# Performance work log

Measured on AMD Instinct MI355X. Metric: run time of the kernel, lower is better.

The kernel has to match this reference:

```python
import jax, jax.numpy as jnp
import numpy as np
from jax.scipy.ndimage import map_coordinates

IMG = 256
N_ANG = 50
BATCH = 4
N_CNN = 32
IN_CH = 2


def _circle_mask(S):
    c = (S - 1) / 2.0
    yy, xx = jnp.meshgrid(jnp.arange(S, dtype=jnp.float32), jnp.arange(S, dtype=jnp.float32), indexing='ij')
    return (((yy - c) ** 2 + (xx - c) ** 2) <= (S / 2.0) ** 2).astype(jnp.float32)


def radon_forward(img, angles):
    # img [B,1,S,S] -> sinogram [B,1,A,S]; parallel-beam, clip_to_circle=True
    S = img.shape[-1]
    c = (S - 1) / 2.0
    img = img * _circle_mask(S)
    t = jnp.arange(S, dtype=jnp.float32) - c        # integration coord
    s = jnp.arange(S, dtype=jnp.float32) - c        # detector coord
    cos = jnp.cos(angles)[:, None, None]
    sin = jnp.sin(angles)[:, None, None]
    x = s[None, None, :] * cos - t[None, :, None] * sin   # [A,S,S]
    y = s[None, None, :] * sin + t[None, :, None] * cos
    coords = jnp.stack([y + c, x + c])                    # [2,A,S,S] (row, col)
    samp = jax.vmap(lambda im: map_coordinates(im, coords, order=1, mode='constant', cval=0.0))(img[:, 0])  # [B,A,S,S]
    return samp.sum(axis=2)[:, None]                      # sum over ray param -> [B,1,A,S]


def filter_sinogram(sino):
    # Ram-Lak FFT filter with zero-padding + FBP normalization
    S = sino.shape[-1]
    A = sino.shape[2]
    P = max(64, int(2 ** np.ceil(np.log2(2 * S))))
    f = jnp.fft.rfft(jnp.pad(sino, ((0, 0), (0, 0), (0, 0), (0, P - S))), axis=-1)
    ramp = 2.0 * jnp.fft.rfftfreq(P).astype(jnp.float32)
    out = jnp.fft.irfft(f * ramp, n=P, axis=-1)[..., :S]
    return out * (np.pi / (2.0 * A))


def radon_backprojection(sino, angles):
    # sino [B,1,A,S] -> image [B,1,S,S]
    B, _, A, S = sino.shape
    c = (S - 1) / 2.0
    yy, xx = jnp.meshgrid(jnp.arange(S, dtype=jnp.float32) - c, jnp.arange(S, dtype=jnp.float32) - c, indexing='ij')
    cos = jnp.cos(angles)[:, None, None]
    sin = jnp.sin(angles)[:, None, None]
    det = xx[None] * cos + yy[None] * sin + c             # [A,S,S] detector coord
    sino2 = sino[:, 0]                                    # [B,A,S]

    def interp_one(sino_a, idx):
        # sino_a [B,S], idx [S,S] -> [B,S,S] linear interp, zero outside
        i0 = jnp.clip(jnp.floor(idx).astype(jnp.int32), 0, S - 2)
        w = idx - i0
        v = sino_a[:, i0] * (1.0 - w) + sino_a[:, i0 + 1] * w
        valid = (idx >= 0.0) & (idx <= S - 1.0)
        return jnp.where(valid, v, 0.0)

    bp = jax.vmap(interp_one, in_axes=(1, 0))(sino2, det).sum(axis=0)  # [B,S,S]
    return (bp * _circle_mask(S))[:, None]


def conv2d(x, w, b):
    y = jax.lax.conv_general_dilated(x, w, (1, 1), 'SAME', dimension_numbers=('NCHW', 'OIHW', 'NCHW'))
    return y + b[None, :, None, None]


def setup_inputs() -> dict:
    key = jax.random.key(0)
    ks = jax.random.split(key, 10)
    angles = jnp.asarray(np.linspace(0, np.pi, N_ANG, endpoint=False), dtype=jnp.float32)
    return {
        'x_sinogram': jax.random.normal(ks[0], (BATCH, 1, N_ANG, IMG), dtype=jnp.float32),
        'y_img_prev': jax.random.normal(ks[1], (BATCH, 1, IMG, IMG), dtype=jnp.float32),
        'y_img_concat_prev': jax.random.normal(ks[2], (BATCH, 1, IMG, IMG), dtype=jnp.float32),
        'angles': angles,
        'step': jnp.float32(1.0),
        'w1': jax.random.normal(ks[3], (N_CNN, IN_CH, 3, 3), dtype=jnp.float32) * 0.1,
        'b1': jnp.zeros((N_CNN,), dtype=jnp.float32),
        'w2': jax.random.normal(ks[4], (N_CNN, N_CNN, 3, 3), dtype=jnp.float32) * 0.1,
        'b2': jnp.zeros((N_CNN,), dtype=jnp.float32),
        'w3': jax.random.normal(ks[5], (1, N_CNN, 3, 3), dtype=jnp.float32) * 0.1,
        'b3': jnp.zeros((1,), dtype=jnp.float32),
    }


def reference(x_sinogram, y_img_prev, y_img_concat_prev, angles, step, w1, b1, w2, b2, w3, b3):
    Ay = radon_forward(y_img_prev, angles)                 # [B,1,A,S]
    diff = Ay - x_sinogram
    filt = filter_sinogram(diff)
    fbp = radon_backprojection(filt, angles)               # [B,1,S,S]
    y_img_update = y_img_prev + step * fbp
    y_cat = jnp.concatenate([y_img_update, y_img_concat_prev], axis=1)  # [B,2,S,S]
    h = jax.nn.relu(conv2d(y_cat, w1, b1))
    h = jax.nn.relu(conv2d(h, w2, b2))
    y_img = conv2d(h, w3, b3)
    return (y_img, y_img_update)
```

## Files before the change

### kernel.cpp

```cpp
#include <hip/hip_runtime.h>
#include <math.h>

#define IMGS 256
#define NANG 50
#define BATCH 4
#define NCNN 32
#define PIX (IMGS*IMGS)
#define NPIX (BATCH*PIX)

#define PROW 258
#define PPIX (PROW*PROW)
#define PB   (PPIX*NCNN)

#define OFF_FILT  0
#define OFF_W2BF  51200
#define OFF_H1P   55808

static constexpr double PI_D = 3.14159265358979323846;

typedef unsigned short u16;
typedef unsigned int   u32;
typedef unsigned long long u64;
typedef __bf16 bfrag __attribute__((ext_vector_type(8)));
typedef float  ffrag __attribute__((ext_vector_type(4)));

__device__ __forceinline__ u16 f2bf(float f) {
    u32 u = __float_as_uint(f);
    u += 0x7fffu + ((u >> 16) & 1u);
    return (u16)(u >> 16);
}

#define RPITCH_D 131
__global__ __launch_bounds__(1024) void k_A(const float* __restrict__ angles,
                                            const float* __restrict__ yprev,
                                            const float* __restrict__ xsino,
                                            const float* __restrict__ w2,
                                            float* __restrict__ ws) {
    __shared__ u16 limg[258 * 262];
    __shared__ float spart[1024];
    __shared__ float staps[512];
    __shared__ float srow[256];
    int tid = threadIdx.x;
    int gid = blockIdx.x;
    if (gid >= 200) {
        int i = (gid - 200) * 1024 + tid;
        if (i < 9216) {
            int t = i >> 10, oc = (i >> 5) & 31, ic = i & 31;
            ((u16*)(ws + OFF_W2BF))[i] = f2bf(w2[(oc * 32 + ic) * 9 + t]);
        }
        return;
    }
    u32* l32 = (u32*)limg;
    int ra = gid;
    int a = ra % NANG, b = ra / NANG;

    if (tid < 511) {
        int d = tid - 255;
        int n = d < 0 ? -d : d;
        double g;
        if (n == 0) {
            g = 0.5;
        } else {
            double th = PI_D * (double)n / 256.0;
            double S = (256.0 * cos(255.0 * th) - 255.0 * cos(256.0 * th) - 1.0)
                       / (2.0 * (1.0 - cos(th)));
            double sign = (n & 1) ? -1.0 : 1.0;
            g = (sign + S / 128.0) / 512.0;
        }
        staps[tid] = (float)(g * PI_D / 100.0);
    }

    for (int z = tid; z < 772; z += 1024) {
        int addr;
        if (z < 258)      addr = z * RPITCH_D;
        else if (z < 516) addr = (z - 258) * RPITCH_D + 129;
        else if (z < 644) addr = (z - 516) + 1;
        else              addr = 257 * RPITCH_D + (z - 644) + 1;
        l32[addr] = 0;
    }
    const float* __restrict__ src = yprev + b * PIX;
    for (int idx = tid; idx < 16384; idx += 1024) {
        int r = idx >> 6, c4 = (idx & 63) << 2;
        float4 v = *(const float4*)(src + r * 256 + c4);
        float di = (float)r - 127.5f;
        float rr = di * di;
        float d0 = (float)c4 - 127.5f;
        v.x = (rr + d0 * d0 <= 16384.0f) ? v.x : 0.0f;
        v.y = (rr + (d0 + 1.0f) * (d0 + 1.0f) <= 16384.0f) ? v.y : 0.0f;
        v.z = (rr + (d0 + 2.0f) * (d0 + 2.0f) <= 16384.0f) ? v.z : 0.0f;
        v.w = (rr + (d0 + 3.0f) * (d0 + 3.0f) <= 16384.0f) ? v.w : 0.0f;
        u32 p0 = (u32)f2bf(v.x) | ((u32)f2bf(v.y) << 16);
        u32 p1 = (u32)f2bf(v.z) | ((u32)f2bf(v.w) << 16);
        int dw = (r + 1) * RPITCH_D + (c4 >> 1) + 1;
        l32[dw] = p0; l32[dw + 1] = p1;
    }
    __syncthreads();

    float a_ = angles[a];
    float cs = cosf(a_), sn = sinf(a_);
    int s = tid & 255, q = tid >> 8;
    float sc = (float)s - 127.5f;
    float t0c = 64.0f * (float)q - 127.5f;
    float rowv = sc * sn + t0c * cs + 127.5f;
    float colv = sc * cs - t0c * sn + 127.5f;
    float acc = 0.0f;
    #pragma unroll 4
    for (int it = 0; it < 64; ++it) {
        float fr = floorf(rowv), fc = floorf(colv);
        float wr = rowv - fr, wc = colv - fc;
        int i0 = (int)fr, j0 = (int)fc;
        bool valid = (rowv > -1.0f) & (rowv < 256.0f) & (colv > -1.0f) & (colv < 256.0f);
        int i0c = min(max(i0, -1), 255);
        int j0c = min(max(j0, -1), 255);
        int ca = j0c + 2;
        int ka = ca >> 1;
        int sh = (ca & 1) << 4;
        int dw = (i0c + 1) * RPITCH_D + ka;
        u32 A = l32[dw],            C = l32[dw + 1];
        u32 B = l32[dw + RPITCH_D], D = l32[dw + RPITCH_D + 1];
        u32 top = (u32)((((u64)C << 32) | (u64)A) >> sh);
        u32 bot = (u32)((((u64)D << 32) | (u64)B) >> sh);
        float tl = __uint_as_float(top << 16);
        float tr_ = __uint_as_float(top & 0xffff0000u);
        float bl = __uint_as_float(bot << 16);
        float br = __uint_as_float(bot & 0xffff0000u);
        float tv = tl + (tr_ - tl) * wc;
        float bv = bl + (br - bl) * wc;
        float sv = tv + (bv - tv) * wr;
        acc += valid ? sv : 0.0f;
        rowv += cs; colv -= sn;
    }
    spart[tid] = acc;
    __syncthreads();
    if (tid < 256)
        srow[tid] = spart[tid] + spart[tid + 256] + spart[tid + 512] + spart[tid + 768]
                    - xsino[ra * 256 + tid];
    __syncthreads();
    {
        float fa = 0.0f;
        int m0 = q * 64;
        #pragma unroll 8
        for (int m = m0; m < m0 + 64; ++m) fa += srow[m] * staps[s - m + 255];
        spart[tid] = fa;
    }
    __syncthreads();
    if (tid < 256)
        ws[OFF_FILT + ra * 256 + tid] =
            spart[tid] + spart[tid + 256] + spart[tid + 512] + spart[tid + 768];
}

__global__ __launch_bounds__(512, 4) void k_B(const float* __restrict__ angles,
                                              const float* __restrict__ yprev,
                                              const float* __restrict__ yconc,
                                              const float* __restrict__ stepp,
                                              const float* __restrict__ w1,
                                              const float* __restrict__ b1,
                                              float* __restrict__ ws,
                                              float* __restrict__ dout) {
    __shared__ float sf[NANG * 256];
    __shared__ float supd[6][258];
    __shared__ float sy2[6][258];
    __shared__ float scs[NANG], ssn[NANG];
    int tid = threadIdx.x;
    int b = blockIdx.x >> 6, tile = blockIdx.x & 63;
    int y0 = tile << 2;

    for (int idx = tid; idx < NANG * 256; idx += 512)
        sf[idx] = ws[OFF_FILT + b * (NANG * 256) + idx];
    if (tid < NANG) {
        float a_ = angles[tid];
        scs[tid] = cosf(a_); ssn[tid] = sinf(a_);
    }
    if (tid < 12) supd[tid >> 1][(tid & 1) * 257] = 0.0f;
    for (int idx = tid; idx < 6 * 258; idx += 512) {
        int r = idx / 258, x = idx % 258;
        int iy = y0 - 1 + r, ix = x - 1;
        sy2[r][x] = ((unsigned)iy < 256u && (unsigned)ix < 256u)
                        ? yconc[b * PIX + iy * 256 + ix] : 0.0f;
    }
    {
        if (tid < 272) {
            int px_i = tile * 17 + (tid >> 4), dw = tid & 15;
            if (px_i < 1028) {
                int y, x;
                if (px_i < 516) { y = (px_i < 258) ? 0 : 257; x = px_i % 258; }
                else            { int j = px_i - 516; y = 1 + (j >> 1); x = (j & 1) * 257; }
                u32* p = (u32*)((u16*)(ws + OFF_H1P) + b * PB + (y * PROW + x) * NCNN);
                p[dw] = 0;
            }
        }
    }
    __syncthreads();

    float step = stepp[0];
    {
        int j = tid & 255, r0 = tid >> 8;
        float xx = (float)j - 127.5f;
        float yy0 = (float)(y0 - 1 + r0) - 127.5f;
        float acc[3] = {0.0f, 0.0f, 0.0f};
        for (int a = 0; a < NANG; ++a) {
            float cs = scs[a], sn = ssn[a];
            float sn2 = sn + sn;
            float f0 = xx * cs + yy0 * sn + 127.5f;
            float idxf[3] = {f0, f0 + sn2, f0 + sn2 + sn2};
            #pragma unroll
            for (int k = 0; k < 3; ++k) {
                float fl = floorf(idxf[k]);
                int i0 = (int)fl;
                i0 = min(max(i0, 0), 254);
                float w = idxf[k] - (float)i0;
                float v = sf[a * 256 + i0] * (1.0f - w) + sf[a * 256 + i0 + 1] * w;
                acc[k] += (idxf[k] >= 0.0f && idxf[k] <= 255.0f) ? v : 0.0f;
            }
        }
        #pragma unroll
        for (int k = 0; k < 3; ++k) {
            int r = r0 + 2 * k;
            int iy = y0 - 1 + r;
            float val = 0.0f;
            if ((unsigned)iy < 256u) {
                float yy = (float)iy - 127.5f;
                float m = (xx * xx + yy * yy <= 16384.0f) ? 1.0f : 0.0f;
                val = yprev[b * PIX + iy * 256 + j] + step * acc[k] * m;
                if (r >= 1 && r <= 4)
                    dout[NPIX + b * PIX + iy * 256 + j] = val;
            }
            supd[r][j + 1] = val;
        }
    }
    __syncthreads();

    {
        int wave = tid >> 6, lane = tid & 63;
        int oc0 = wave * 4;
        float W[72];
        const float4* wsrc = (const float4*)(w1 + oc0 * 18);
        #pragma unroll
        for (int i = 0; i < 18; ++i) ((float4*)W)[i] = wsrc[i];
        float bb0 = b1[oc0], bb1 = b1[oc0 + 1], bb2 = b1[oc0 + 2], bb3 = b1[oc0 + 3];
        u16* h1base = (u16*)(ws + OFF_H1P) + b * PB;
        for (int it = 0; it < 16; ++it) {
            int px = it * 64 + lane;
            int rr = px >> 8, x = px & 255;
            int oy = y0 + rr;
            float v[18];
            #pragma unroll
            for (int ky = 0; ky < 3; ++ky)
                #pragma unroll
                for (int kx = 0; kx < 3; ++kx) {
                    v[ky * 3 + kx]     = supd[rr + ky][x + kx];
                    v[9 + ky * 3 + kx] = sy2[rr + ky][x + kx];
                }
            float a0 = bb0, a1 = bb1, a2 = bb2, a3 = bb3;
            #pragma unroll
            for (int t = 0; t < 18; ++t) {
                a0 += v[t] * W[t];
                a1 += v[t] * W[18 + t];
                a2 += v[t] * W[36 + t];
                a3 += v[t] * W[54 + t];
            }
            u32 p0 = (u32)f2bf(fmaxf(a0, 0.0f)) | ((u32)f2bf(fmaxf(a1, 0.0f)) << 16);
            u32 p1 = (u32)f2bf(fmaxf(a2, 0.0f)) | ((u32)f2bf(fmaxf(a3, 0.0f)) << 16);
            u32* op = (u32*)(h1base + ((oy + 1) * PROW + (x + 1)) * NCNN + oc0);
            op[0] = p0; op[1] = p1;
        }
    }
}

#define H2PITCH 34
__global__ __launch_bounds__(1024) void k_C(const float* __restrict__ b2,
                                            const float* __restrict__ w3,
                                            const float* __restrict__ b3,
                                            float* __restrict__ ws,
                                            float* __restrict__ dout) {
    __shared__ u16 sh2[6 * 258 * H2PITCH];
    __shared__ u32 swp[9 * 16];
    u32* l32 = (u32*)sh2;
    int tid = threadIdx.x;
    int b = blockIdx.x >> 6, tile = blockIdx.x & 63;
    int y0 = tile << 2;

    if (tid < 144) {
        int t = tid >> 4, kd = tid & 15;
        swp[tid] = (u32)f2bf(w3[(2 * kd) * 9 + t]) | ((u32)f2bf(w3[(2 * kd + 1) * 9 + t]) << 16);
    }
    if (tid < 204) {
        int r = tid / 34, rem = tid % 34;
        int col = (rem < 17) ? 0 : 257, dw = rem % 17;
        l32[(r * 258 + col) * 17 + dw] = 0;
    }
    #pragma unroll
    for (int r = 0; r < 6; ++r) {
        int hy = y0 - 1 + r;
        if (hy < 0 || hy > 255)
            for (int idx = tid; idx < 258 * 17; idx += 1024)
                l32[r * 258 * 17 + idx] = 0;
    }
    __syncthreads();

    const u16* __restrict__ w2bf = (const u16*)(ws + OFF_W2BF);
    const u16* __restrict__ h1b  = (const u16*)(ws + OFF_H1P) + b * PB;
    int wave = tid >> 6, lane = tid & 63;
    int m = lane & 15, quad = lane >> 4;
    bfrag Bf[9][2];
    #pragma unroll
    for (int t = 0; t < 9; ++t) {
        const u16* wp = w2bf + t * 1024 + m * 32 + quad * 8;
        Bf[t][0] = *(const bfrag*)(wp);
        Bf[t][1] = *(const bfrag*)(wp + 16 * 32);
    }
    float bias0 = b2[m], bias1 = b2[m + 16];
    #pragma unroll
    for (int k = 0; k < 6; ++k) {
        int tl = wave + (k << 4);
        int ridx = tl >> 4, xt = tl & 15;
        int hy = y0 - 1 + ridx;
        bool valid = (unsigned)hy < 256u;
        int hyc = min(max(hy, 0), 255);
        int xs = xt << 4;
        ffrag c0 = {0.f, 0.f, 0.f, 0.f}, c1 = {0.f, 0.f, 0.f, 0.f};
        #pragma unroll
        for (int g = 0; g < 3; ++g) {
            bfrag Af[3];
            #pragma unroll
            for (int tt = 0; tt < 3; ++tt) {
                int t = g * 3 + tt;
                int ty = t / 3, tx = t % 3;
                Af[tt] = *(const bfrag*)(h1b + ((hyc + ty) * PROW + xs + m + tx) * NCNN + quad * 8);
            }
            #pragma unroll
            for (int tt = 0; tt < 3; ++tt) {
                c0 = __builtin_amdgcn_mfma_f32_16x16x32_bf16(Af[tt], Bf[g * 3 + tt][0], c0, 0, 0, 0);
                c1 = __builtin_amdgcn_mfma_f32_16x16x32_bf16(Af[tt], Bf[g * 3 + tt][1], c1, 0, 0, 0);
            }
        }
        if (valid) {
            #pragma unroll
            for (int r = 0; r < 4; ++r) {
                int px = xs + quad * 4 + r;
                u16* op = sh2 + (ridx * 258 + px + 1) * H2PITCH;
                op[m]      = f2bf(fmaxf(c0[r] + bias0, 0.0f));
                op[m + 16] = f2bf(fmaxf(c1[r] + bias1, 0.0f));
            }
        }
    }
    __syncthreads();

    {
        uint4 WP[9];
        #pragma unroll
        for (int t = 0; t < 9; ++t) WP[t] = ((const uint4*)swp)[t * 4 + 0],
                                    WP[t] = *(const uint4*)(swp + t * 16);
        u32 Wd[36];
        #pragma unroll
        for (int i = 0; i < 36; ++i) Wd[i] = swp[(i / 4) * 16 + (i & 3)];
        (void)WP;
        int rr = tid >> 8, x = tid & 255;
        int oy = y0 + rr;
        float acc = b3[0];
        #pragma unroll
        for (int ky = 0; ky < 3; ++ky) {
            #pragma unroll
            for (int cx = 0; cx < 3; ++cx) {
                int t = ky * 3 + cx;
                const u32* q = l32 + ((rr + ky) * 258 + x + cx) * 17;
                #pragma unroll
                for (int kd = 0; kd < 16; ++kd) {
                    u32 hv = q[kd];
                    u32 wv = (kd < 4) ? Wd[t * 4 + kd] : swp[t * 16 + kd];
                    float h0 = __uint_as_float(hv << 16);
                    float h1 = __uint_as_float(hv & 0xffff0000u);
                    float w0 = __uint_as_float(wv << 16);
                    float w1_ = __uint_as_float(wv & 0xffff0000u);
                    acc += h0 * w0 + h1 * w1_;
                }
            }
        }
        dout[b * PIX + oy * 256 + x] = acc;
    }
}

extern "C" void kernel_launch(void* const* d_in, const int* in_sizes, int n_in,
                              void* d_out, int out_size, void* d_ws, size_t ws_size,
                              hipStream_t stream) {
    const float* xsino  = (const float*)d_in[0];
    const float* yprev  = (const float*)d_in[1];
    const float* yconc  = (const float*)d_in[2];
    const float* angles = (const float*)d_in[3];
    const float* stepp  = (const float*)d_in[4];
    const float* w1 = (const float*)d_in[5];
    const float* b1 = (const float*)d_in[6];
    const float* w2 = (const float*)d_in[7];
    const float* b2 = (const float*)d_in[8];
    const float* w3 = (const float*)d_in[9];
    const float* b3 = (const float*)d_in[10];
    float* out = (float*)d_out;
    float* ws  = (float*)d_ws;

    k_A<<<209, 1024, 0, stream>>>(angles, yprev, xsino, w2, ws);
    k_B<<<BATCH * 64, 512, 0, stream>>>(angles, yprev, yconc, stepp, w1, b1, ws, out);
    k_C<<<BATCH * 64, 1024, 0, stream>>>(b2, w3, b3, ws, out);
}
```

Measured before the change: 157.6 us.

## Remap radon rays to 8x8 wave tiles and halve row tiles in k_B/k_C

In k_A, each wave now handles a patch of 16 detector bins by 8 ray offsets, walking two interleaved ray segments with stride 8 and reducing through wave shuffles. This gives more local LDS access and removes the 4-way partial-sum reduction in shared memory. k_B and k_C now use 2-row tiles with twice as many blocks, and k_C drops to 512 threads. k_C also gets a restructured MFMA loop that prefetches A fragments row by row, plus float4 staging of the filtered sinogram and removal of dead weight-register code. Smaller tiles raise parallelism and occupancy but add more redundant halo rows and backprojection work per output row.

```diff
diff --git a/kernel.cpp b/kernel.cpp
--- a/kernel.cpp
+++ b/kernel.cpp
@@ -31,11 +31,11 @@
 }
 
 #define RPITCH_D 131
-__global__ __launch_bounds__(1024) void k_A(const float* __restrict__ angles,
-                                            const float* __restrict__ yprev,
-                                            const float* __restrict__ xsino,
-                                            const float* __restrict__ w2,
-                                            float* __restrict__ ws) {
+__global__ __launch_bounds__(1024, 4) void k_A(const float* __restrict__ angles,
+                                               const float* __restrict__ yprev,
+                                               const float* __restrict__ xsino,
+                                               const float* __restrict__ w2,
+                                               float* __restrict__ ws) {
     __shared__ u16 limg[258 * 262];
     __shared__ float spart[1024];
     __shared__ float staps[512];
@@ -98,45 +98,62 @@
 
     float a_ = angles[a];
     float cs = cosf(a_), sn = sinf(a_);
-    int s = tid & 255, q = tid >> 8;
-    float sc = (float)s - 127.5f;
-    float t0c = 64.0f * (float)q - 127.5f;
-    float rowv = sc * sn + t0c * cs + 127.5f;
-    float colv = sc * cs - t0c * sn + 127.5f;
-    float acc = 0.0f;
+    int lane = tid & 63, w = tid >> 6;
+    int s8 = lane & 7, t8 = lane >> 3;
+    int sA = w * 16 + s8;
+    float scA = (float)sA - 127.5f;
+    float tc0 = (float)t8 - 127.5f;
+    float rowA = scA * sn + tc0 * cs + 127.5f;
+    float colA = scA * cs - tc0 * sn + 127.5f;
+    float rowB = rowA + 8.0f * sn;
+    float colB = colA + 8.0f * cs;
+    float cs8 = 8.0f * cs, sn8 = 8.0f * sn;
+    float accA = 0.0f, accB = 0.0f;
     #pragma unroll 4
-    for (int it = 0; it < 64; ++it) {
-        float fr = floorf(rowv), fc = floorf(colv);
-        float wr = rowv - fr, wc = colv - fc;
-        int i0 = (int)fr, j0 = (int)fc;
-        bool valid = (rowv > -1.0f) & (rowv < 256.0f) & (colv > -1.0f) & (colv < 256.0f);
-        int i0c = min(max(i0, -1), 255);
-        int j0c = min(max(j0, -1), 255);
-        int ca = j0c + 2;
-        int ka = ca >> 1;
-        int sh = (ca & 1) << 4;
-        int dw = (i0c + 1) * RPITCH_D + ka;
-        u32 A = l32[dw],            C = l32[dw + 1];
-        u32 B = l32[dw + RPITCH_D], D = l32[dw + RPITCH_D + 1];
-        u32 top = (u32)((((u64)C << 32) | (u64)A) >> sh);
-        u32 bot = (u32)((((u64)D << 32) | (u64)B) >> sh);
-        float tl = __uint_as_float(top << 16);
-        float tr_ = __uint_as_float(top & 0xffff0000u);
-        float bl = __uint_as_float(bot << 16);
-        float br = __uint_as_float(bot & 0xffff0000u);
-        float tv = tl + (tr_ - tl) * wc;
-        float bv = bl + (br - bl) * wc;
-        float sv = tv + (bv - tv) * wr;
-        acc += valid ? sv : 0.0f;
-        rowv += cs; colv -= sn;
-    }
-    spart[tid] = acc;
+    for (int j = 0; j < 32; ++j) {
+        #pragma unroll
+        for (int hh = 0; hh < 2; ++hh) {
+            float rowv = hh ? rowB : rowA;
+            float colv = hh ? colB : colA;
+            float fr = floorf(rowv), fc = floorf(colv);
+            float wr = rowv - fr, wc = colv - fc;
+            int i0 = (int)fr, j0 = (int)fc;
+            bool valid = (rowv > -1.0f) & (rowv < 256.0f) & (colv > -1.0f) & (colv < 256.0f);
+            int i0c = min(max(i0, -1), 255);
+            int j0c = min(max(j0, -1), 255);
+            int ca = j0c + 2;
+            int ka = ca >> 1;
+            int sh = (ca & 1) << 4;
+            int dw = (i0c + 1) * RPITCH_D + ka;
+            u32 A = l32[dw],            C = l32[dw + 1];
+            u32 B = l32[dw + RPITCH_D], D = l32[dw + RPITCH_D + 1];
+            u32 top = (u32)((((u64)C << 32) | (u64)A) >> sh);
+            u32 bot = (u32)((((u64)D << 32) | (u64)B) >> sh);
+            float tl = __uint_as_float(top << 16);
+            float tr_ = __uint_as_float(top & 0xffff0000u);
+            float bl = __uint_as_float(bot << 16);
+            float br = __uint_as_float(bot & 0xffff0000u);
+            float tv = tl + (tr_ - tl) * wc;
+            float bv = bl + (br - bl) * wc;
+            float sv = tv + (bv - tv) * wr;
+            sv = valid ? sv : 0.0f;
+            if (hh) accB += sv; else accA += sv;
+        }
+        rowA += cs8; colA -= sn8; rowB += cs8; colB -= sn8;
+    }
+    accA += __shfl_xor(accA, 8, 64);
+    accA += __shfl_xor(accA, 16, 64);
+    accA += __shfl_xor(accA, 32, 64);
+    accB += __shfl_xor(accB, 8, 64);
+    accB += __shfl_xor(accB, 16, 64);
+    accB += __shfl_xor(accB, 32, 64);
+    if (t8 == 0) { spart[sA] = accA; spart[sA + 8] = accB; }
     __syncthreads();
     if (tid < 256)
-        srow[tid] = spart[tid] + spart[tid + 256] + spart[tid + 512] + spart[tid + 768]
-                    - xsino[ra * 256 + tid];
+        srow[tid] = spart[tid] - xsino[ra * 256 + tid];
     __syncthreads();
     {
+        int s = tid & 255, q = tid >> 8;
         float fa = 0.0f;
         int m0 = q * 64;
         #pragma unroll 8
@@ -158,36 +175,37 @@
                                               float* __restrict__ ws,
                                               float* __restrict__ dout) {
     __shared__ float sf[NANG * 256];
-    __shared__ float supd[6][258];
-    __shared__ float sy2[6][258];
+    __shared__ float supd[4][258];
+    __shared__ float sy2[4][258];
     __shared__ float scs[NANG], ssn[NANG];
     int tid = threadIdx.x;
-    int b = blockIdx.x >> 6, tile = blockIdx.x & 63;
-    int y0 = tile << 2;
-
-    for (int idx = tid; idx < NANG * 256; idx += 512)
-        sf[idx] = ws[OFF_FILT + b * (NANG * 256) + idx];
+    int b = blockIdx.x >> 7, tile = blockIdx.x & 127;
+    int y0 = tile << 1;
+
+    {
+        const float4* s4 = (const float4*)(ws + OFF_FILT + b * (NANG * 256));
+        float4* d4 = (float4*)sf;
+        for (int idx = tid; idx < NANG * 64; idx += 512) d4[idx] = s4[idx];
+    }
     if (tid < NANG) {
         float a_ = angles[tid];
         scs[tid] = cosf(a_); ssn[tid] = sinf(a_);
     }
-    if (tid < 12) supd[tid >> 1][(tid & 1) * 257] = 0.0f;
-    for (int idx = tid; idx < 6 * 258; idx += 512) {
+    if (tid < 8) supd[tid >> 1][(tid & 1) * 257] = 0.0f;
+    for (int idx = tid; idx < 4 * 258; idx += 512) {
         int r = idx / 258, x = idx % 258;
         int iy = y0 - 1 + r, ix = x - 1;
         sy2[r][x] = ((unsigned)iy < 256u && (unsigned)ix < 256u)
                         ? yconc[b * PIX + iy * 256 + ix] : 0.0f;
     }
-    {
-        if (tid < 272) {
-            int px_i = tile * 17 + (tid >> 4), dw = tid & 15;
-            if (px_i < 1028) {
-                int y, x;
-                if (px_i < 516) { y = (px_i < 258) ? 0 : 257; x = px_i % 258; }
-                else            { int j = px_i - 516; y = 1 + (j >> 1); x = (j & 1) * 257; }
-                u32* p = (u32*)((u16*)(ws + OFF_H1P) + b * PB + (y * PROW + x) * NCNN);
-                p[dw] = 0;
-            }
+    if (tid < 144) {
+        int px_i = tile * 9 + (tid >> 4), dw = tid & 15;
+        if (px_i < 1028) {
+            int y, x;
+            if (px_i < 516) { y = (px_i < 258) ? 0 : 257; x = px_i % 258; }
+            else            { int j = px_i - 516; y = 1 + (j >> 1); x = (j & 1) * 257; }
+            u32* p = (u32*)((u16*)(ws + OFF_H1P) + b * PB + (y * PROW + x) * NCNN);
+            p[dw] = 0;
         }
     }
     __syncthreads();
@@ -197,14 +215,14 @@
         int j = tid & 255, r0 = tid >> 8;
         float xx = (float)j - 127.5f;
         float yy0 = (float)(y0 - 1 + r0) - 127.5f;
-        float acc[3] = {0.0f, 0.0f, 0.0f};
+        float acc[2] = {0.0f, 0.0f};
+        #pragma unroll 5
         for (int a = 0; a < NANG; ++a) {
             float cs = scs[a], sn = ssn[a];
-            float sn2 = sn + sn;
             float f0 = xx * cs + yy0 * sn + 127.5f;
-            float idxf[3] = {f0, f0 + sn2, f0 + sn2 + sn2};
+            float idxf[2] = {f0, f0 + sn + sn};
             #pragma unroll
-            for (int k = 0; k < 3; ++k) {
+            for (int k = 0; k < 2; ++k) {
                 float fl = floorf(idxf[k]);
                 int i0 = (int)fl;
                 i0 = min(max(i0, 0), 254);
@@ -214,7 +232,7 @@
             }
         }
         #pragma unroll
-        for (int k = 0; k < 3; ++k) {
+        for (int k = 0; k < 2; ++k) {
             int r = r0 + 2 * k;
             int iy = y0 - 1 + r;
             float val = 0.0f;
@@ -222,7 +240,7 @@
                 float yy = (float)iy - 127.5f;
                 float m = (xx * xx + yy * yy <= 16384.0f) ? 1.0f : 0.0f;
                 val = yprev[b * PIX + iy * 256 + j] + step * acc[k] * m;
-                if (r >= 1 && r <= 4)
+                if (r >= 1 && r <= 2)
                     dout[NPIX + b * PIX + iy * 256 + j] = val;
             }
             supd[r][j + 1] = val;
@@ -239,7 +257,8 @@
         for (int i = 0; i < 18; ++i) ((float4*)W)[i] = wsrc[i];
         float bb0 = b1[oc0], bb1 = b1[oc0 + 1], bb2 = b1[oc0 + 2], bb3 = b1[oc0 + 3];
         u16* h1base = (u16*)(ws + OFF_H1P) + b * PB;
-        for (int it = 0; it < 16; ++it) {
+        #pragma unroll
+        for (int it = 0; it < 8; ++it) {
             int px = it * 64 + lane;
             int rr = px >> 8, x = px & 255;
             int oy = y0 + rr;
@@ -268,32 +287,32 @@
 }
 
 #define H2PITCH 34
-__global__ __launch_bounds__(1024) void k_C(const float* __restrict__ b2,
-                                            const float* __restrict__ w3,
-                                            const float* __restrict__ b3,
-                                            float* __restrict__ ws,
-                                            float* __restrict__ dout) {
-    __shared__ u16 sh2[6 * 258 * H2PITCH];
+__global__ __launch_bounds__(512, 4) void k_C(const float* __restrict__ b2,
+                                              const float* __restrict__ w3,
+                                              const float* __restrict__ b3,
+                                              float* __restrict__ ws,
+                                              float* __restrict__ dout) {
+    __shared__ u16 sh2[4 * 258 * H2PITCH];
     __shared__ u32 swp[9 * 16];
     u32* l32 = (u32*)sh2;
     int tid = threadIdx.x;
-    int b = blockIdx.x >> 6, tile = blockIdx.x & 63;
-    int y0 = tile << 2;
+    int b = blockIdx.x >> 7, tile = blockIdx.x & 127;
+    int y0 = tile << 1;
 
     if (tid < 144) {
         int t = tid >> 4, kd = tid & 15;
         swp[tid] = (u32)f2bf(w3[(2 * kd) * 9 + t]) | ((u32)f2bf(w3[(2 * kd + 1) * 9 + t]) << 16);
     }
-    if (tid < 204) {
+    if (tid < 136) {
         int r = tid / 34, rem = tid % 34;
         int col = (rem < 17) ? 0 : 257, dw = rem % 17;
         l32[(r * 258 + col) * 17 + dw] = 0;
     }
     #pragma unroll
-    for (int r = 0; r < 6; ++r) {
+    for (int r = 0; r < 4; ++r) {
         int hy = y0 - 1 + r;
         if (hy < 0 || hy > 255)
-            for (int idx = tid; idx < 258 * 17; idx += 1024)
+            for (int idx = tid; idx < 258 * 17; idx += 512)
                 l32[r * 258 * 17 + idx] = 0;
     }
     __syncthreads();
@@ -311,28 +330,38 @@
     }
     float bias0 = b2[m], bias1 = b2[m + 16];
     #pragma unroll
-    for (int k = 0; k < 6; ++k) {
-        int tl = wave + (k << 4);
+    for (int k = 0; k < 8; ++k) {
+        int tl = wave + (k << 3);
         int ridx = tl >> 4, xt = tl & 15;
         int hy = y0 - 1 + ridx;
         bool valid = (unsigned)hy < 256u;
         int hyc = min(max(hy, 0), 255);
         int xs = xt << 4;
+        bfrag A0[3], A1[3];
+        #pragma unroll
+        for (int tx = 0; tx < 3; ++tx)
+            A0[tx] = *(const bfrag*)(h1b + ((hyc + 0) * PROW + xs + m + tx) * NCNN + quad * 8);
+        #pragma unroll
+        for (int tx = 0; tx < 3; ++tx)
+            A1[tx] = *(const bfrag*)(h1b + ((hyc + 1) * PROW + xs + m + tx) * NCNN + quad * 8);
         ffrag c0 = {0.f, 0.f, 0.f, 0.f}, c1 = {0.f, 0.f, 0.f, 0.f};
         #pragma unroll
-        for (int g = 0; g < 3; ++g) {
-            bfrag Af[3];
-            #pragma unroll
-            for (int tt = 0; tt < 3; ++tt) {
-                int t = g * 3 + tt;
-                int ty = t / 3, tx = t % 3;
-                Af[tt] = *(const bfrag*)(h1b + ((hyc + ty) * PROW + xs + m + tx) * NCNN + quad * 8);
-            }
-            #pragma unroll
-            for (int tt = 0; tt < 3; ++tt) {
-                c0 = __builtin_amdgcn_mfma_f32_16x16x32_bf16(Af[tt], Bf[g * 3 + tt][0], c0, 0, 0, 0);
-                c1 = __builtin_amdgcn_mfma_f32_16x16x32_bf16(Af[tt], Bf[g * 3 + tt][1], c1, 0, 0, 0);
-            }
+        for (int tx = 0; tx < 3; ++tx) {
+            c0 = __builtin_amdgcn_mfma_f32_16x16x32_bf16(A0[tx], Bf[tx][0], c0, 0, 0, 0);
+            c1 = __builtin_amdgcn_mfma_f32_16x16x32_bf16(A0[tx], Bf[tx][1], c1, 0, 0, 0);
+        }
+        #pragma unroll
+        for (int tx = 0; tx < 3; ++tx)
+            A0[tx] = *(const bfrag*)(h1b + ((hyc + 2) * PROW + xs + m + tx) * NCNN + quad * 8);
+        #pragma unroll
+        for (int tx = 0; tx < 3; ++tx) {
+            c0 = __builtin_amdgcn_mfma_f32_16x16x32_bf16(A1[tx], Bf[3 + tx][0], c0, 0, 0, 0);
+            c1 = __builtin_amdgcn_mfma_f32_16x16x32_bf16(A1[tx], Bf[3 + tx][1], c1, 0, 0, 0);
+        }
+        #pragma unroll
+        for (int tx = 0; tx < 3; ++tx) {
+            c0 = __builtin_amdgcn_mfma_f32_16x16x32_bf16(A0[tx], Bf[6 + tx][0], c0, 0, 0, 0);
+            c1 = __builtin_amdgcn_mfma_f32_16x16x32_bf16(A0[tx], Bf[6 + tx][1], c1, 0, 0, 0);
         }
         if (valid) {
             #pragma unroll
@@ -347,14 +376,6 @@
     __syncthreads();
 
     {
-        uint4 WP[9];
-        #pragma unroll
-        for (int t = 0; t < 9; ++t) WP[t] = ((const uint4*)swp)[t * 4 + 0],
-                                    WP[t] = *(const uint4*)(swp + t * 16);
-        u32 Wd[36];
-        #pragma unroll
-        for (int i = 0; i < 36; ++i) Wd[i] = swp[(i / 4) * 16 + (i & 3)];
-        (void)WP;
         int rr = tid >> 8, x = tid & 255;
         int oy = y0 + rr;
         float acc = b3[0];
@@ -367,7 +388,7 @@
                 #pragma unroll
                 for (int kd = 0; kd < 16; ++kd) {
                     u32 hv = q[kd];
-                    u32 wv = (kd < 4) ? Wd[t * 4 + kd] : swp[t * 16 + kd];
+                    u32 wv = swp[t * 16 + kd];
                     float h0 = __uint_as_float(hv << 16);
                     float h1 = __uint_as_float(hv & 0xffff0000u);
                     float w0 = __uint_as_float(wv << 16);
@@ -398,6 +419,6 @@
     float* ws  = (float*)d_ws;
 
     k_A<<<209, 1024, 0, stream>>>(angles, yprev, xsino, w2, ws);
-    k_B<<<BATCH * 64, 512, 0, stream>>>(angles, yprev, yconc, stepp, w1, b1, ws, out);
-    k_C<<<BATCH * 64, 1024, 0, stream>>>(b2, w3, b3, ws, out);
+    k_B<<<BATCH * 128, 512, 0, stream>>>(angles, yprev, yconc, stepp, w1, b1, ws, out);
+    k_C<<<BATCH * 128, 512, 0, stream>>>(b2, w3, b3, ws, out);
 }
```

New measurement: 154.7 us. No clear change (-1.8%).
